# Kernel tuning notes

Hardware: AMD Instinct MI355X
Metric: run time of the kernel (lower is better)

Reference implementation:

```python
import jax, jax.numpy as jnp
import numpy as np

H_HEADS = 4
C_HID = 128
N_GENE = 50000
N_DIS = 25000
F_GENE = 512
F_DIS = 256
E1 = 150000
E2 = 150000
BN_EPS = 1e-5


def _encode(x, W, b, gamma, beta):
    # Linear -> ReLU -> (dropout off) -> BatchNorm1d (train-mode batch stats, biased var)
    h = jax.nn.relu(x @ W + b)
    mu = h.mean(axis=0)
    var = h.var(axis=0)
    return gamma * (h - mu) * jax.lax.rsqrt(var + BN_EPS) + beta


def _with_self_loops(src, dst, n_loop):
    # PyG GATConv: remove_self_loops (mask src==dst) then add_self_loops(num_nodes=min(Ns,Nd))
    loop = jnp.arange(n_loop, dtype=src.dtype)
    mask = jnp.concatenate([src != dst, jnp.ones((n_loop,), bool)])
    return jnp.concatenate([src, loop]), jnp.concatenate([dst, loop]), mask


def _gat(x_src, x_dst, src, dst, mask, Ws, Wd, a_s, a_d, bias, n_dst):
    H, C = a_s.shape
    xs = (x_src @ Ws).reshape(-1, H, C)  # [Ns,H,C]
    xd = (x_dst @ Wd).reshape(-1, H, C)  # [Nd,H,C]
    ls = jnp.sum(xs * a_s, axis=-1)      # [Ns,H]
    ld = jnp.sum(xd * a_d, axis=-1)      # [Nd,H]
    logits = jax.nn.leaky_relu(ls[src] + ld[dst], 0.2)  # [E,H]
    logits = jnp.where(mask[:, None], logits, jnp.asarray(-1e30, logits.dtype))
    m = jax.ops.segment_max(logits, dst, num_segments=n_dst)
    m = jnp.where(jnp.isfinite(m), m, 0.0)  # empty segments -> -inf fill
    p = jnp.exp(logits - m[dst]) * mask[:, None]
    denom = jax.ops.segment_sum(p, dst, num_segments=n_dst)[dst]
    alpha = p / jnp.where(denom > 0, denom, 1.0)  # softmax per destination
    out = jax.ops.segment_sum(alpha[:, :, None] * xs[src], dst, num_segments=n_dst)
    return out.mean(axis=1) + bias  # concat=False: mean over heads


def _forward(x_gene, x_dis, e1_src, e1_dst, e2_src, e2_dst,
             Wg, bg, gg, betag, Wd, bd, gd, betad,
             W1s, W1d, a1s, a1d, b1, W2s, W2d, a2s, a2d, b2):
    gene = _encode(x_gene, Wg, bg, gg, betag)
    dis = _encode(x_dis, Wd, bd, gd, betad)
    # relation 1: Disease -> Gene (bipartite); self loops use min(N_dis, N_gene)
    s1, d1, m1 = _with_self_loops(e1_src, e1_dst, min(N_DIS, N_GENE))
    gene = gene + _gat(dis, gene, s1, d1, m1, W1s, W1d, a1s, a1d, b1, N_GENE)
    # relation 2: Gene -> Gene (uses updated gene features)
    s2, d2, m2 = _with_self_loops(e2_src, e2_dst, N_GENE)
    gene = gene + _gat(gene, gene, s2, d2, m2, W2s, W2d, a2s, a2d, b2, N_GENE)
    # output_layer is skipped: gene dim (128) != hidden*heads (512)
    return gene, dis


def setup_inputs() -> dict:
    key = jax.random.key(0)
    ks = jax.random.split(key, 24)
    H, C = H_HEADS, C_HID

    def glorot(k, shape):
        fan = shape[0] + shape[-1]
        return jax.random.normal(k, shape, jnp.float32) * np.sqrt(2.0 / fan).astype(np.float32)

    return {
        'x_gene': jax.random.normal(ks[0], (N_GENE, F_GENE), jnp.float32),
        'x_dis': jax.random.normal(ks[1], (N_DIS, F_DIS), jnp.float32),
        'e1_src': jax.random.randint(ks[2], (E1,), 0, N_DIS, jnp.int32),
        'e1_dst': jax.random.randint(ks[3], (E1,), 0, N_GENE, jnp.int32),
        'e2_src': jax.random.randint(ks[4], (E2,), 0, N_GENE, jnp.int32),
        'e2_dst': jax.random.randint(ks[5], (E2,), 0, N_GENE, jnp.int32),
        'Wg': glorot(ks[6], (F_GENE, C)), 'bg': jnp.zeros(C), 'gg': jnp.ones(C), 'betag': jnp.zeros(C),
        'Wd': glorot(ks[7], (F_DIS, C)), 'bd': jnp.zeros(C), 'gd': jnp.ones(C), 'betad': jnp.zeros(C),
        'W1s': glorot(ks[8], (C, H * C)), 'W1d': glorot(ks[9], (C, H * C)),
        'a1s': glorot(ks[10], (H, C)), 'a1d': glorot(ks[11], (H, C)), 'b1': jnp.zeros(C),
        'W2s': glorot(ks[12], (C, H * C)), 'W2d': glorot(ks[13], (C, H * C)),
        'a2s': glorot(ks[14], (H, C)), 'a2d': glorot(ks[15], (H, C)), 'b2': jnp.zeros(C),
    }


def reference(x_gene, x_dis, e1_src, e1_dst, e2_src, e2_dst,
              Wg, bg, gg, betag, Wd, bd, gd, betad,
              W1s, W1d, a1s, a1d, b1, W2s, W2d, a2s, a2d, b2):
    return _forward(x_gene, x_dis, e1_src, e1_dst, e2_src, e2_dst,
                    Wg, bg, gg, betag, Wd, bd, gd, betad,
                    W1s, W1d, a1s, a1d, b1, W2s, W2d, a2s, a2d, b2)
```

## Files before the change

kernel.cpp:

```cpp
#include <hip/hip_runtime.h>
#include <hip/hip_bf16.h>
#include <math.h>

#define N_GENE 50000
#define N_DIS  25000
#define F_GENE 512
#define F_DIS  256
#define E_EDGES 150000
#define BN_EPS 1e-5f

typedef unsigned short u16;
typedef unsigned int u32;
typedef short s16x8 __attribute__((ext_vector_type(8)));
typedef float f32x4 __attribute__((ext_vector_type(4)));

__device__ __forceinline__ u16 f2bf(float f) {
    union { float f; unsigned u; } c; c.f = f;
    unsigned u = c.u;
    unsigned rounding = 0x7FFFu + ((u >> 16) & 1u);
    return (u16)((u + rounding) >> 16);
}
__device__ __forceinline__ void load_bf16x8(const u16* p, float* f) {
    uint4 q = *reinterpret_cast<const uint4*>(p);
    unsigned w0 = q.x, w1 = q.y, w2 = q.z, w3 = q.w;
    f[0] = __uint_as_float(w0 << 16); f[1] = __uint_as_float(w0 & 0xffff0000u);
    f[2] = __uint_as_float(w1 << 16); f[3] = __uint_as_float(w1 & 0xffff0000u);
    f[4] = __uint_as_float(w2 << 16); f[5] = __uint_as_float(w2 & 0xffff0000u);
    f[6] = __uint_as_float(w3 << 16); f[7] = __uint_as_float(w3 & 0xffff0000u);
}

__device__ __forceinline__ void gload_lds16(const u16* g, u16* l) {
    __builtin_amdgcn_global_load_lds(
        (const __attribute__((address_space(1))) u32*)g,
        (__attribute__((address_space(3))) u32*)l, 16, 0, 0);
}

__device__ __forceinline__ void pack_one(const float* __restrict__ W, u16* __restrict__ Bp,
                                         int K, int N, int i) {
    int K8 = K >> 3;
    int n = i / K8, ko = i - n * K8;
    int k0 = ko * 8;
    int nt = n >> 4, mr = n & 15, kc = k0 >> 5, quad = (k0 >> 3) & 3;
    u16 tmp[8];
#pragma unroll
    for (int j = 0; j < 8; j++) tmp[j] = f2bf(W[(size_t)(k0 + j) * N + n]);
    *reinterpret_cast<uint4*>(&Bp[((size_t)(nt * (K >> 5) + kc) * 64 + quad * 16 + mr) * 8]) =
        *reinterpret_cast<const uint4*>(tmp);
}

__global__ void prep(const float* __restrict__ Wg, const float* __restrict__ Wd,
                     const float* __restrict__ W1s, const float* __restrict__ W2s,
                     u16* __restrict__ Wgt, u16* __restrict__ Wdt,
                     u16* __restrict__ W1st, u16* __restrict__ W2st,
                     float* __restrict__ stats_g, float* __restrict__ stats_d,
                     int* __restrict__ deg1, int* __restrict__ deg2,
                     const float* __restrict__ W1d, const float* __restrict__ a1d,
                     const float* __restrict__ W2d, const float* __restrict__ a2d,
                     float* __restrict__ weff) {
    int i = blockIdx.x * 256 + threadIdx.x;
    if (i < 8192) { pack_one(Wg, Wgt, 512, 128, i); return; }
    i -= 8192;
    if (i < 4096) { pack_one(Wd, Wdt, 256, 128, i); return; }
    i -= 4096;
    if (i < 8192) { pack_one(W1s, W1st, 128, 512, i); return; }
    i -= 8192;
    if (i < 8192) { pack_one(W2s, W2st, 128, 512, i); return; }
    i -= 8192;
    if (i < 256) { stats_g[i] = 0.f; return; }
    i -= 256;
    if (i < 256) { stats_d[i] = 0.f; return; }
    i -= 256;
    if (i < N_GENE) { deg1[i] = 0; return; }
    i -= N_GENE;
    if (i < N_GENE) { deg2[i] = 0; return; }
    i -= N_GENE;
    if (i < 1024) {
        int rel = i >> 9, tt = i & 511;
        int h = tt >> 7, k = tt & 127;
        const float* Wp = rel ? W2d : W1d;
        const float* ap = rel ? a2d : a1d;
        float s = 0.f;
        for (int c = 0; c < 128; c++) s += Wp[k * 512 + h * 128 + c] * ap[h * 128 + c];
        weff[rel * 512 + h * 128 + k] = s;
    }
}

template <int K, bool A_FRAG, bool RELU_BIAS, bool OUT_BF16, bool FUSE_STATS, bool FUSE_LS>
__global__ __launch_bounds__(256) void gemm_lds(const void* __restrict__ Ap,
                                                const u16* __restrict__ Bp,
                                                const float* __restrict__ bias,
                                                void* __restrict__ outp, int M, int NFULL,
                                                float* __restrict__ stats,
                                                const float* __restrict__ as_,
                                                float* __restrict__ ls_out) {
    constexpr int KC = K / 32;
    constexpr int CK = 2;
    constexpr int NCH = KC / CK;
    __shared__ u16 Bs[2][8 * CK * 64 * 8];
    __shared__ float sstat[256];
    const int wave = threadIdx.x >> 6;
    const int lane = threadIdx.x & 63;
    const int mrow = lane & 15;
    const int quad = lane >> 4;
    const int m0 = (blockIdx.x * 4 + wave) * 16;
    const int n0 = blockIdx.y * 128;
    const int arow = (m0 + mrow < M) ? m0 + mrow : M - 1;
    const int rt = (m0 >> 4) < ((M + 15) >> 4) ? (m0 >> 4) : ((M + 15) >> 4) - 1;
    const u16* bslab = Bp + (size_t)(n0 >> 4) * KC * 512;

    if constexpr (FUSE_STATS) sstat[threadIdx.x] = 0.f;

    f32x4 acc[8];
#pragma unroll
    for (int t = 0; t < 8; t++) acc[t] = (f32x4){0.f, 0.f, 0.f, 0.f};

    struct ARegs { float4 f[2 * CK]; s16x8 s[CK]; };
    ARegs A0, A1;

    auto stageB = [&](int c, int b) {
#pragma unroll
        for (int q = 0; q < 2 * CK; q++) {
            int fi = wave * 2 * CK + q;
            int t = fi / CK, kcp = fi % CK;
            const u16* g = bslab + ((size_t)(t * KC + c * CK + kcp) * 64 + lane) * 8;
            gload_lds16(g, &Bs[b][(size_t)fi * 512]);
        }
    };
    auto loadA = [&](int c, ARegs& A) {
        if constexpr (A_FRAG) {
#pragma unroll
            for (int kcp = 0; kcp < CK; kcp++)
                A.s[kcp] = *reinterpret_cast<const s16x8*>(
                    (const u16*)Ap + ((size_t)(rt * KC + c * CK + kcp) * 64 + lane) * 8);
        } else {
#pragma unroll
            for (int kcp = 0; kcp < CK; kcp++) {
                const float* ap = (const float*)Ap + (size_t)arow * K + (c * CK + kcp) * 32 + quad * 8;
                A.f[2 * kcp]     = *reinterpret_cast<const float4*>(ap);
                A.f[2 * kcp + 1] = *reinterpret_cast<const float4*>(ap + 4);
            }
        }
    };
    auto compute = [&](const u16* Bsb, const ARegs& A) {
#pragma unroll
        for (int kcp = 0; kcp < CK; kcp++) {
            s16x8 af;
            if constexpr (A_FRAG) {
                af = A.s[kcp];
            } else {
                const float4 lo = A.f[2 * kcp], hi = A.f[2 * kcp + 1];
                af[0] = (short)f2bf(lo.x); af[1] = (short)f2bf(lo.y);
                af[2] = (short)f2bf(lo.z); af[3] = (short)f2bf(lo.w);
                af[4] = (short)f2bf(hi.x); af[5] = (short)f2bf(hi.y);
                af[6] = (short)f2bf(hi.z); af[7] = (short)f2bf(hi.w);
            }
#pragma unroll
            for (int t = 0; t < 8; t++) {
                const s16x8 bfr = *reinterpret_cast<const s16x8*>(
                    &Bsb[((size_t)(t * CK + kcp) * 64 + lane) * 8]);
                acc[t] = __builtin_amdgcn_mfma_f32_16x16x32_bf16(af, bfr, acc[t], 0, 0, 0);
            }
        }
    };

#define FENCE_N() do { if constexpr (A_FRAG) asm volatile("s_waitcnt vmcnt(6)" ::: "memory"); \
                       else                  asm volatile("s_waitcnt vmcnt(8)" ::: "memory"); } while (0)
#define FENCE_0() asm volatile("s_waitcnt vmcnt(0)" ::: "memory")
#define LGKM0()   asm volatile("s_waitcnt lgkmcnt(0)" ::: "memory")
#define BAR()     asm volatile("s_barrier" ::: "memory")

    stageB(0, 0);
    loadA(0, A0);
    for (int cc = 0; cc < NCH / 2; ++cc) {
        stageB(2 * cc + 1, 1);
        loadA(2 * cc + 1, A1);
        FENCE_N();
        BAR();
        compute(&Bs[0][0], A0);
        LGKM0();
        BAR();
        if (cc + 1 < NCH / 2) {
            stageB(2 * cc + 2, 0);
            loadA(2 * cc + 2, A0);
            FENCE_N();
        } else {
            FENCE_0();
        }
        BAR();
        compute(&Bs[1][0], A1);
        LGKM0();
        BAR();
    }
#undef FENCE_N
#undef FENCE_0
#undef LGKM0
#undef BAR

    float asv[8];
    if constexpr (FUSE_LS) {
        const int h = blockIdx.y;
#pragma unroll
        for (int t = 0; t < 8; t++) asv[t] = as_[h * 128 + t * 16 + mrow];
    }
    float lsp[4] = {0.f, 0.f, 0.f, 0.f};

#pragma unroll
    for (int t = 0; t < 8; t++) {
        int col = n0 + t * 16 + mrow;
        float sv = 0.f, sv2 = 0.f;
#pragma unroll
        for (int r = 0; r < 4; r++) {
            int orow = m0 + quad * 4 + r;
            if (orow < M) {
                float v = acc[t][r];
                if (RELU_BIAS) v = fmaxf(v + bias[col], 0.f);
                if (OUT_BF16)
                    ((u16*)outp)[(size_t)orow * NFULL + col] = f2bf(v);
                else
                    ((float*)outp)[(size_t)orow * NFULL + col] = v;
                if constexpr (FUSE_STATS) { sv += v; sv2 += v * v; }
                if constexpr (FUSE_LS) lsp[r] += v * asv[t];
            }
        }
        if constexpr (FUSE_STATS) {
            sv  += __shfl_xor(sv, 16, 64);  sv  += __shfl_xor(sv, 32, 64);
            sv2 += __shfl_xor(sv2, 16, 64); sv2 += __shfl_xor(sv2, 32, 64);
            if (quad == 0) {
                atomicAdd(&sstat[t * 16 + mrow], sv);
                atomicAdd(&sstat[128 + t * 16 + mrow], sv2);
            }
        }
    }
    if constexpr (FUSE_LS) {
        const int h = blockIdx.y;
#pragma unroll
        for (int r = 0; r < 4; r++) {
            float p = lsp[r];
            p += __shfl_xor(p, 1, 64); p += __shfl_xor(p, 2, 64);
            p += __shfl_xor(p, 4, 64); p += __shfl_xor(p, 8, 64);
            int orow = m0 + quad * 4 + r;
            if (mrow == 0 && orow < M) ls_out[orow * 4 + h] = p;
        }
    }
    if constexpr (FUSE_STATS) {
        __syncthreads();
        atomicAdd(&stats[threadIdx.x], sstat[threadIdx.x]);
    }
}

__global__ void bn_apply(float* __restrict__ X, const float* __restrict__ stats,
                         const float* __restrict__ gamma, const float* __restrict__ beta,
                         u16* __restrict__ mirror, const float* __restrict__ weff,
                         float* __restrict__ ld_out, int M) {
    int i = blockIdx.x * 256 + threadIdx.x;
    if (i >= M * 16) return;
    int row = i >> 4, cg = i & 15;
    float inv_m = 1.0f / (float)M;
    float4 lo = *reinterpret_cast<const float4*>(&X[(size_t)row * 128 + cg * 8]);
    float4 hi = *reinterpret_cast<const float4*>(&X[(size_t)row * 128 + cg * 8 + 4]);
    float v[8] = {lo.x, lo.y, lo.z, lo.w, hi.x, hi.y, hi.z, hi.w};
    u16 mb[8];
#pragma unroll
    for (int e = 0; e < 8; e++) {
        int col = cg * 8 + e;
        float mu = stats[col] * inv_m;
        float var = stats[128 + col] * inv_m - mu * mu;
        v[e] = gamma[col] * (v[e] - mu) * rsqrtf(var + BN_EPS) + beta[col];
        mb[e] = f2bf(v[e]);
    }
    *reinterpret_cast<float4*>(&X[(size_t)row * 128 + cg * 8]) = (float4){v[0], v[1], v[2], v[3]};
    *reinterpret_cast<float4*>(&X[(size_t)row * 128 + cg * 8 + 4]) = (float4){v[4], v[5], v[6], v[7]};
    if (mirror) {
        int kc = cg >> 2, quad = cg & 3, ml = quad * 16 + (row & 15), rt = row >> 4;
        *reinterpret_cast<uint4*>(&mirror[((size_t)(rt * 4 + kc) * 64 + ml) * 8]) =
            *reinterpret_cast<const uint4*>(mb);
    }
    if (ld_out) {
#pragma unroll
        for (int h = 0; h < 4; h++) {
            float p = 0.f;
#pragma unroll
            for (int e = 0; e < 8; e++) p += v[e] * weff[h * 128 + cg * 8 + e];
            p += __shfl_xor(p, 1, 64); p += __shfl_xor(p, 2, 64);
            p += __shfl_xor(p, 4, 64); p += __shfl_xor(p, 8, 64);
            if (cg == 0) ld_out[row * 4 + h] = p;
        }
    }
}

__global__ void count_both(const int* __restrict__ e1s, const int* __restrict__ e1d,
                           const int* __restrict__ e2s, const int* __restrict__ e2d,
                           int* __restrict__ deg1, int* __restrict__ deg2) {
    int i = blockIdx.x * 256 + threadIdx.x;
    if (i < E_EDGES + N_DIS) {
        int d;
        if (i < E_EDGES) { int s = e1s[i]; d = e1d[i]; if (s == d) return; }
        else d = i - E_EDGES;
        atomicAdd(&deg1[d], 1);
        return;
    }
    i -= E_EDGES + N_DIS;
    if (i < E_EDGES + N_GENE) {
        int d;
        if (i < E_EDGES) { int s = e2s[i]; d = e2d[i]; if (s == d) return; }
        else d = i - E_EDGES;
        atomicAdd(&deg2[d], 1);
    }
}

__global__ __launch_bounds__(1024) void scan_both(const int* __restrict__ deg1, int* __restrict__ offs1, int* __restrict__ cur1,
                                                  const int* __restrict__ deg2, int* __restrict__ offs2, int* __restrict__ cur2) {
    const int* deg = blockIdx.x ? deg2 : deg1;
    int* offs = blockIdx.x ? offs2 : offs1;
    int* cur  = blockIdx.x ? cur2  : cur1;
    const int n = N_GENE;
    __shared__ int sh[1024];
    int tid = threadIdx.x;
    const int chunk = (n + 1023) >> 10;
    int base = tid * chunk;
    int s = 0;
    for (int j = 0; j < chunk; j++) { int i = base + j; if (i < n) s += deg[i]; }
    sh[tid] = s;
    __syncthreads();
    for (int off = 1; off < 1024; off <<= 1) {
        int t = (tid >= off) ? sh[tid - off] : 0;
        __syncthreads();
        sh[tid] += t;
        __syncthreads();
    }
    int ex = tid ? sh[tid - 1] : 0;
    for (int j = 0; j < chunk; j++) {
        int i = base + j;
        if (i < n) { offs[i] = ex; cur[i] = ex; ex += deg[i]; }
    }
    if (tid == 1023) offs[n] = sh[1023];
}

__global__ void scatter_both(const int* __restrict__ e1s, const int* __restrict__ e1d,
                             const int* __restrict__ e2s, const int* __restrict__ e2d,
                             int* __restrict__ cur1, int* __restrict__ cur2,
                             int* __restrict__ esrc1, int* __restrict__ esrc2) {
    int i = blockIdx.x * 256 + threadIdx.x;
    if (i < E_EDGES + N_DIS) {
        int s, d;
        if (i < E_EDGES) { s = e1s[i]; d = e1d[i]; if (s == d) return; }
        else { s = i - E_EDGES; d = s; }
        esrc1[atomicAdd(&cur1[d], 1)] = s;
        return;
    }
    i -= E_EDGES + N_DIS;
    if (i < E_EDGES + N_GENE) {
        int s, d;
        if (i < E_EDGES) { s = e2s[i]; d = e2d[i]; if (s == d) return; }
        else { s = i - E_EDGES; d = s; }
        esrc2[atomicAdd(&cur2[d], 1)] = s;
    }
}

__global__ void gat_kernel(const int* __restrict__ offs, const int* __restrict__ esrc,
                           const float* __restrict__ ls, const float* __restrict__ ld,
                           const u16* __restrict__ xs, const float* __restrict__ bias,
                           float* __restrict__ xdst_out, u16* __restrict__ mirror,
                           const float* __restrict__ weff2, float* __restrict__ ld2_out,
                           int n_dst) {
    int wid = (blockIdx.x * blockDim.x + threadIdx.x) >> 6;
    int lane = threadIdx.x & 63;
    if (wid >= n_dst) return;
    int h = lane >> 4;
    int beg = offs[wid], end = offs[wid + 1];
    float ldv = ld[wid * 4 + h];
    float m = -INFINITY;
    for (int j = beg; j < end; j++) {
        int s = esrc[j];
        float l = ls[s * 4 + h] + ldv;
        l = l > 0.f ? l : 0.2f * l;
        m = fmaxf(m, l);
    }
    float denom = 0.f;
    float acc[8] = {0.f, 0.f, 0.f, 0.f, 0.f, 0.f, 0.f, 0.f};
    for (int j = beg; j < end; j++) {
        int s = esrc[j];
        float l = ls[s * 4 + h] + ldv;
        l = l > 0.f ? l : 0.2f * l;
        float p = __expf(l - m);
        denom += p;
        float xv[8];
        load_bf16x8(xs + (size_t)s * 512 + lane * 8, xv);
        #pragma unroll
        for (int k = 0; k < 8; k++) acc[k] += p * xv[k];
    }
    float dinv = denom > 0.f ? 1.f / denom : 1.f;
    #pragma unroll
    for (int k = 0; k < 8; k++) {
        float v = acc[k] * dinv;
        v += __shfl_xor(v, 16, 64);
        v += __shfl_xor(v, 32, 64);
        acc[k] = v * 0.25f;
    }
    if (lane < 16) {
        int c0 = lane * 8;
        float vout[8];
        #pragma unroll
        for (int k = 0; k < 8; k++) {
            vout[k] = xdst_out[(size_t)wid * 128 + c0 + k] + acc[k] + bias[c0 + k];
            xdst_out[(size_t)wid * 128 + c0 + k] = vout[k];
        }
        if (mirror) {
            unsigned pk[4];
            #pragma unroll
            for (int kk = 0; kk < 4; kk++)
                pk[kk] = (unsigned)f2bf(vout[2 * kk]) | ((unsigned)f2bf(vout[2 * kk + 1]) << 16);
            int kc = lane >> 2, quad = lane & 3, ml = quad * 16 + (wid & 15), rt = wid >> 4;
            *reinterpret_cast<uint4*>(&mirror[((size_t)(rt * 4 + kc) * 64 + ml) * 8]) =
                *reinterpret_cast<const uint4*>(pk);
        }
        if (weff2) {
            #pragma unroll
            for (int hh = 0; hh < 4; hh++) {
                float p = 0.f;
                #pragma unroll
                for (int k = 0; k < 8; k++) p += vout[k] * weff2[hh * 128 + c0 + k];
                p += __shfl_xor(p, 1, 64); p += __shfl_xor(p, 2, 64);
                p += __shfl_xor(p, 4, 64); p += __shfl_xor(p, 8, 64);
                if (lane == 0) ld2_out[wid * 4 + hh] = p;
            }
        }
    }
}

static inline int cdiv(int a, int b) { return (a + b - 1) / b; }

extern "C" void kernel_launch(void* const* d_in, const int* in_sizes, int n_in,
                              void* d_out, int out_size, void* d_ws, size_t ws_size,
                              hipStream_t stream) {
    const float* x_gene = (const float*)d_in[0];
    const float* x_dis  = (const float*)d_in[1];
    const int* e1s = (const int*)d_in[2];
    const int* e1d = (const int*)d_in[3];
    const int* e2s = (const int*)d_in[4];
    const int* e2d = (const int*)d_in[5];
    const float *Wg = (const float*)d_in[6],  *bg = (const float*)d_in[7];
    const float *gg = (const float*)d_in[8],  *betag = (const float*)d_in[9];
    const float *Wd = (const float*)d_in[10], *bd = (const float*)d_in[11];
    const float *gd = (const float*)d_in[12], *betad = (const float*)d_in[13];
    const float *W1s = (const float*)d_in[14], *W1d = (const float*)d_in[15];
    const float *a1s = (const float*)d_in[16], *a1d = (const float*)d_in[17];
    const float *b1  = (const float*)d_in[18];
    const float *W2s = (const float*)d_in[19], *W2d = (const float*)d_in[20];
    const float *a2s = (const float*)d_in[21], *a2d = (const float*)d_in[22];
    const float *b2  = (const float*)d_in[23];

    float* gene_f = (float*)d_out;
    float* dis_f  = (float*)d_out + (size_t)N_GENE * 128;

    char* p = (char*)d_ws;
    auto alloc = [&](size_t bytes) {
        char* r = p;
        p += (bytes + 255) & ~(size_t)255;
        return r;
    };
    u16*   xs_buf  = (u16*)  alloc((size_t)N_GENE * 512 * 2);
    u16*   gene_bf = (u16*)  alloc((size_t)cdiv(N_GENE, 16) * 2048 * 2);
    u16*   dis_bf  = (u16*)  alloc((size_t)cdiv(N_DIS, 16) * 2048 * 2);
    float* ls_buf  = (float*)alloc((size_t)N_GENE * 4 * 4);
    float* ld1_buf = (float*)alloc((size_t)N_GENE * 4 * 4);
    float* ld2_buf = (float*)alloc((size_t)N_GENE * 4 * 4);
    float* weff    = (float*)alloc(1024 * 4);
    float* stats_g = (float*)alloc(256 * 4);
    float* stats_d = (float*)alloc(256 * 4);
    int*   deg1    = (int*)  alloc((size_t)N_GENE * 4);
    int*   deg2    = (int*)  alloc((size_t)N_GENE * 4);
    int*   offs1   = (int*)  alloc((size_t)(N_GENE + 1) * 4);
    int*   offs2   = (int*)  alloc((size_t)(N_GENE + 1) * 4);
    int*   cur1    = (int*)  alloc((size_t)N_GENE * 4);
    int*   cur2    = (int*)  alloc((size_t)N_GENE * 4);
    int*   esrc1   = (int*)  alloc((size_t)(E_EDGES + N_GENE) * 4);
    int*   esrc2   = (int*)  alloc((size_t)(E_EDGES + N_GENE) * 4);
    u16*   Wgt  = (u16*)alloc((size_t)8 * 16 * 512 * 2);
    u16*   Wdt  = (u16*)alloc((size_t)8 * 8 * 512 * 2);
    u16*   W1st = (u16*)alloc((size_t)32 * 4 * 512 * 2);
    u16*   W2st = (u16*)alloc((size_t)32 * 4 * 512 * 2);

    const int PREP_T = 8192 + 4096 + 8192 + 8192 + 256 + 256 + N_GENE + N_GENE + 1024;
    prep<<<cdiv(PREP_T, 256), 256, 0, stream>>>(Wg, Wd, W1s, W2s, Wgt, Wdt, W1st, W2st,
                                                stats_g, stats_d, deg1, deg2,
                                                W1d, a1d, W2d, a2d, weff);
    const int EB = cdiv((E_EDGES + N_DIS) + (E_EDGES + N_GENE), 256);
    count_both<<<EB, 256, 0, stream>>>(e1s, e1d, e2s, e2d, deg1, deg2);
    scan_both<<<2, 1024, 0, stream>>>(deg1, offs1, cur1, deg2, offs2, cur2);
    scatter_both<<<EB, 256, 0, stream>>>(e1s, e1d, e2s, e2d, cur1, cur2, esrc1, esrc2);

    gemm_lds<512, false, true, false, true, false><<<dim3(cdiv(N_GENE, 64), 1), 256, 0, stream>>>(
        x_gene, Wgt, bg, gene_f, N_GENE, 128, stats_g, nullptr, nullptr);
    bn_apply<<<cdiv(N_GENE * 16, 256), 256, 0, stream>>>(gene_f, stats_g, gg, betag,
                                                         nullptr, weff, ld1_buf, N_GENE);

    gemm_lds<256, false, true, false, true, false><<<dim3(cdiv(N_DIS, 64), 1), 256, 0, stream>>>(
        x_dis, Wdt, bd, dis_f, N_DIS, 128, stats_d, nullptr, nullptr);
    bn_apply<<<cdiv(N_DIS * 16, 256), 256, 0, stream>>>(dis_f, stats_d, gd, betad,
                                                        dis_bf, nullptr, nullptr, N_DIS);

    gemm_lds<128, true, false, true, false, true><<<dim3(cdiv(N_DIS, 64), 4), 256, 0, stream>>>(
        dis_bf, W1st, nullptr, xs_buf, N_DIS, 512, nullptr, a1s, ls_buf);
    gat_kernel<<<cdiv(N_GENE, 4), 256, 0, stream>>>(offs1, esrc1, ls_buf, ld1_buf, xs_buf, b1,
                                                    gene_f, gene_bf, weff + 512, ld2_buf, N_GENE);

    gemm_lds<128, true, false, true, false, true><<<dim3(cdiv(N_GENE, 64), 4), 256, 0, stream>>>(
        gene_bf, W2st, nullptr, xs_buf, N_GENE, 512, nullptr, a2s, ls_buf);
    gat_kernel<<<cdiv(N_GENE, 4), 256, 0, stream>>>(offs2, esrc2, ls_buf, ld2_buf, xs_buf, b2,
                                                    gene_f, nullptr, nullptr, nullptr, N_GENE);
}
```

Before: 593.1 us.

## Replace two-block CSR offset scan with a three-pass multi-block scan

The exclusive prefix sum over node degrees used to run in just two 1024-thread blocks, one per relation, each thread scanning a strided chunk serially. It now runs as three kernels: per-block reductions, a scan of the block sums, and a final per-block scan that adds the block offset. This spreads the work across many CUs instead of two, at the cost of two extra kernel launches and another pass over the degree arrays. The 256-entry block-sum scan fits NB=196.

```diff
diff --git a/kernel.cpp b/kernel.cpp
--- a/kernel.cpp
+++ b/kernel.cpp
@@ -308,32 +308,62 @@
     }
 }
 
-__global__ __launch_bounds__(1024) void scan_both(const int* __restrict__ deg1, int* __restrict__ offs1, int* __restrict__ cur1,
-                                                  const int* __restrict__ deg2, int* __restrict__ offs2, int* __restrict__ cur2) {
-    const int* deg = blockIdx.x ? deg2 : deg1;
-    int* offs = blockIdx.x ? offs2 : offs1;
-    int* cur  = blockIdx.x ? cur2  : cur1;
-    const int n = N_GENE;
-    __shared__ int sh[1024];
+__global__ void block_sum_both(const int* __restrict__ deg1, const int* __restrict__ deg2,
+                               int* __restrict__ bsum, int nb) {
+    __shared__ int sh[256];
+    int rel = blockIdx.x >= nb;
+    int blk = rel ? blockIdx.x - nb : blockIdx.x;
+    const int* deg = rel ? deg2 : deg1;
+    int i = blk * 256 + threadIdx.x;
+    sh[threadIdx.x] = (i < N_GENE) ? deg[i] : 0;
+    __syncthreads();
+    for (int s = 128; s > 0; s >>= 1) {
+        if (threadIdx.x < s) sh[threadIdx.x] += sh[threadIdx.x + s];
+        __syncthreads();
+    }
+    if (threadIdx.x == 0) bsum[blockIdx.x] = sh[0];
+}
+
+__global__ void scan_bsum_both(int* __restrict__ bsum, int nb,
+                               int* __restrict__ offs1, int* __restrict__ offs2) {
+    __shared__ int sh[256];
+    int* bs = bsum + blockIdx.x * nb;
     int tid = threadIdx.x;
-    const int chunk = (n + 1023) >> 10;
-    int base = tid * chunk;
-    int s = 0;
-    for (int j = 0; j < chunk; j++) { int i = base + j; if (i < n) s += deg[i]; }
-    sh[tid] = s;
+    int v = (tid < nb) ? bs[tid] : 0;
+    sh[tid] = v;
     __syncthreads();
-    for (int off = 1; off < 1024; off <<= 1) {
+    for (int off = 1; off < 256; off <<= 1) {
         int t = (tid >= off) ? sh[tid - off] : 0;
         __syncthreads();
         sh[tid] += t;
         __syncthreads();
     }
-    int ex = tid ? sh[tid - 1] : 0;
-    for (int j = 0; j < chunk; j++) {
-        int i = base + j;
-        if (i < n) { offs[i] = ex; cur[i] = ex; ex += deg[i]; }
-    }
-    if (tid == 1023) offs[n] = sh[1023];
+    if (tid < nb) bs[tid] = sh[tid] - v;
+    if (tid == 255) (blockIdx.x ? offs2 : offs1)[N_GENE] = sh[255];
+}
+
+__global__ void scan_final_both(const int* __restrict__ deg1, const int* __restrict__ deg2,
+                                const int* __restrict__ bsum, int nb,
+                                int* __restrict__ offs1, int* __restrict__ cur1,
+                                int* __restrict__ offs2, int* __restrict__ cur2) {
+    __shared__ int sh[256];
+    int rel = blockIdx.x >= nb;
+    int blk = rel ? blockIdx.x - nb : blockIdx.x;
+    const int* deg = rel ? deg2 : deg1;
+    int* offs = rel ? offs2 : offs1;
+    int* cur  = rel ? cur2  : cur1;
+    int i = blk * 256 + threadIdx.x, tid = threadIdx.x;
+    int v = (i < N_GENE) ? deg[i] : 0;
+    sh[tid] = v;
+    __syncthreads();
+    for (int off = 1; off < 256; off <<= 1) {
+        int t = (tid >= off) ? sh[tid - off] : 0;
+        __syncthreads();
+        sh[tid] += t;
+        __syncthreads();
+    }
+    int ex = bsum[blockIdx.x] + sh[tid] - v;
+    if (i < N_GENE) { offs[i] = ex; cur[i] = ex; }
 }
 
 __global__ void scatter_both(const int* __restrict__ e1s, const int* __restrict__ e1d,
@@ -474,6 +504,7 @@
     int*   offs2   = (int*)  alloc((size_t)(N_GENE + 1) * 4);
     int*   cur1    = (int*)  alloc((size_t)N_GENE * 4);
     int*   cur2    = (int*)  alloc((size_t)N_GENE * 4);
+    int*   bsum    = (int*)  alloc(512 * 4);
     int*   esrc1   = (int*)  alloc((size_t)(E_EDGES + N_GENE) * 4);
     int*   esrc2   = (int*)  alloc((size_t)(E_EDGES + N_GENE) * 4);
     u16*   Wgt  = (u16*)alloc((size_t)8 * 16 * 512 * 2);
@@ -481,13 +512,17 @@
     u16*   W1st = (u16*)alloc((size_t)32 * 4 * 512 * 2);
     u16*   W2st = (u16*)alloc((size_t)32 * 4 * 512 * 2);
 
+    const int NB = cdiv(N_GENE, 256);
+
     const int PREP_T = 8192 + 4096 + 8192 + 8192 + 256 + 256 + N_GENE + N_GENE + 1024;
     prep<<<cdiv(PREP_T, 256), 256, 0, stream>>>(Wg, Wd, W1s, W2s, Wgt, Wdt, W1st, W2st,
                                                 stats_g, stats_d, deg1, deg2,
                                                 W1d, a1d, W2d, a2d, weff);
     const int EB = cdiv((E_EDGES + N_DIS) + (E_EDGES + N_GENE), 256);
     count_both<<<EB, 256, 0, stream>>>(e1s, e1d, e2s, e2d, deg1, deg2);
-    scan_both<<<2, 1024, 0, stream>>>(deg1, offs1, cur1, deg2, offs2, cur2);
+    block_sum_both<<<2 * NB, 256, 0, stream>>>(deg1, deg2, bsum, NB);
+    scan_bsum_both<<<2, 256, 0, stream>>>(bsum, NB, offs1, offs2);
+    scan_final_both<<<2 * NB, 256, 0, stream>>>(deg1, deg2, bsum, NB, offs1, cur1, offs2, cur2);
     scatter_both<<<EB, 256, 0, stream>>>(e1s, e1d, e2s, e2d, cur1, cur2, esrc1, esrc2);
 
     gemm_lds<512, false, true, false, true, false><<<dim3(cdiv(N_GENE, 64), 1), 256, 0, stream>>>(
```

Measured after the change: 476.5 us. -19.7%, faster.
